# Kernel tuning notes

Hardware: AMD Instinct MI355X
Metric: run time of the kernel (lower is better)

## Reference

```python
import jax, jax.numpy as jnp
import numpy as np

TEMP = 0.5

def setup_inputs() -> dict:
    key = jax.random.key(0)
    k1, k2 = jax.random.split(key)
    B, D = 4096, 256
    x_i = jax.random.normal(k1, (B, D), dtype=jnp.float32)
    x_j = jax.random.normal(k2, (B, D), dtype=jnp.float32)
    return {"x_i": x_i, "x_j": x_j}

def reference(x_i, x_j):
    B = x_i.shape[0]
    z = jnp.concatenate([x_i, x_j], axis=0)  # [2B, D]
    # cosine similarity = normalized dot product (eps matches torch default 1e-8)
    zn = z / jnp.maximum(jnp.linalg.norm(z, axis=-1, keepdims=True), 1e-8)
    sim = zn @ zn.T  # [2B, 2B]
    sim_ij = jnp.diagonal(sim, offset=B)
    sim_ji = jnp.diagonal(sim, offset=-B)
    pos = jnp.concatenate([sim_ij, sim_ji], axis=0)  # [2B]
    # neg_mask = ~eye: zero out self-similarity in the denominator
    exp_sim = jnp.exp(sim / TEMP)
    idx = jnp.arange(2 * B)
    denom = jnp.sum(exp_sim, axis=1) - exp_sim[idx, idx]  # masked row-sum
    loss = jnp.sum(-(pos / TEMP - jnp.log(denom))) / (2 * B)
    return loss
```

## Files before the change

kernel.cpp:

```cpp
#include <hip/hip_runtime.h>
#include <stdint.h>

#define B_ROWS 4096
#define D 256
#define NTOT (2 * B_ROWS)
#define NSPLIT 16
#define BM 256
#define COLS_PER_BLOCK (NTOT / NSPLIT)
#define JT_COUNT (COLS_PER_BLOCK / 64)
#define C_SCALE 2.8853900817779268f

typedef __attribute__((ext_vector_type(8))) short bf16x8;
typedef __attribute__((ext_vector_type(4))) float f32x4;
typedef __attribute__((ext_vector_type(4))) unsigned short us4;

typedef const __attribute__((address_space(1))) char gch;
typedef __attribute__((address_space(3))) char lch;

static __device__ __forceinline__ unsigned short f2bf(float f) {
  union { float f; unsigned u; } v; v.f = f;
  unsigned r = v.u + 0x7FFFu + ((v.u >> 16) & 1u);
  return (unsigned short)(r >> 16);
}

__global__ __launch_bounds__(256) void k_prep(const float* __restrict__ xi,
                                              const float* __restrict__ xj,
                                              unsigned short* __restrict__ zn,
                                              unsigned short* __restrict__ zns,
                                              float* __restrict__ pos,
                                              float* __restrict__ out) {
  if (blockIdx.x == 0 && threadIdx.x == 0) out[0] = 0.0f;
  int p = blockIdx.x * 4 + (threadIdx.x >> 6);
  int lane = threadIdx.x & 63;
  float4 a = ((const float4*)(xi + (size_t)p * D))[lane];
  float4 b = ((const float4*)(xj + (size_t)p * D))[lane];
  float sa = a.x * a.x + a.y * a.y + a.z * a.z + a.w * a.w;
  float sb = b.x * b.x + b.y * b.y + b.z * b.z + b.w * b.w;
  float ab = a.x * b.x + a.y * b.y + a.z * b.z + a.w * b.w;
  #pragma unroll
  for (int m = 1; m < 64; m <<= 1) {
    sa += __shfl_xor(sa, m, 64);
    sb += __shfl_xor(sb, m, 64);
    ab += __shfl_xor(ab, m, 64);
  }
  float ia = 1.0f / fmaxf(sqrtf(sa), 1e-8f);
  float ib = 1.0f / fmaxf(sqrtf(sb), 1e-8f);
  float na[4] = {a.x * ia, a.y * ia, a.z * ia, a.w * ia};
  float nb[4] = {b.x * ib, b.y * ib, b.z * ib, b.w * ib};
  us4 oa, ob, sa4, sb4;
  oa.x = f2bf(na[0]); oa.y = f2bf(na[1]); oa.z = f2bf(na[2]); oa.w = f2bf(na[3]);
  ob.x = f2bf(nb[0]); ob.y = f2bf(nb[1]); ob.z = f2bf(nb[2]); ob.w = f2bf(nb[3]);
  sa4.x = f2bf(na[0] * C_SCALE); sa4.y = f2bf(na[1] * C_SCALE);
  sa4.z = f2bf(na[2] * C_SCALE); sa4.w = f2bf(na[3] * C_SCALE);
  sb4.x = f2bf(nb[0] * C_SCALE); sb4.y = f2bf(nb[1] * C_SCALE);
  sb4.z = f2bf(nb[2] * C_SCALE); sb4.w = f2bf(nb[3] * C_SCALE);
  *(us4*)(zn  + (size_t)p * D + lane * 4) = oa;
  *(us4*)(zn  + (size_t)(p + B_ROWS) * D + lane * 4) = ob;
  *(us4*)(zns + (size_t)p * D + lane * 4) = sa4;
  *(us4*)(zns + (size_t)(p + B_ROWS) * D + lane * 4) = sb4;
  if (lane == 0) {
    float d = ab * ia * ib;
    pos[p] = d;
    pos[p + B_ROWS] = d;
  }
}

__global__ __launch_bounds__(512, 4) void k_gemm(const unsigned short* __restrict__ zn,
                                                 const unsigned short* __restrict__ zns,
                                                 float* __restrict__ part) {
  __shared__ char lds[2 * 32768];
  int rb = (int)(blockIdx.x / NSPLIT) * BM;
  int cs = (int)(blockIdx.x % NSPLIT);
  int cb = cs * COLS_PER_BLOCK;
  int w = threadIdx.x >> 6;
  int lane = threadIdx.x & 63;
  int hi = lane >> 4, lo = lane & 15;

  const char* znb  = (const char*)zn;
  const char* znsb = (const char*)zns;

  bf16x8 a0[8], a1[8];
  int r0 = rb + w * 32 + lo;
  #pragma unroll
  for (int f = 0; f < 8; f++) {
    a0[f] = *(const bf16x8*)(znsb + (size_t)r0 * 512 + f * 64 + hi * 16);
    a1[f] = *(const bf16x8*)(znsb + (size_t)(r0 + 16) * 512 + f * 64 + hi * 16);
  }

  int rdbase[8];
  #pragma unroll
  for (int f = 0; f < 8; f++)
    rdbase[f] = lo * 512 + ((f * 64 + hi * 16) ^ ((lo & 7) << 4));

  float rs[2][4] = {{0.f, 0.f, 0.f, 0.f}, {0.f, 0.f, 0.f, 0.f}};

  auto stage = [&](int bufofs, int colrow) {
    #pragma unroll
    for (int c = 0; c < 4; c++) {
      int local = w * 4096 + c * 1024 + lane * 16;
      int src = local ^ (((local >> 9) & 7) << 4);
      __builtin_amdgcn_global_load_lds(
          (gch*)(znb + (size_t)colrow * 512 + src),
          (lch*)(lds + bufofs + w * 4096 + c * 1024), 16, 0, 0);
    }
  };
  auto compute = [&](int bufofs) {
    #pragma unroll
    for (int nt = 0; nt < 4; nt++) {
      f32x4 acc0 = {0.f, 0.f, 0.f, 0.f}, acc1 = {0.f, 0.f, 0.f, 0.f};
      #pragma unroll
      for (int f = 0; f < 8; f++) {
        bf16x8 b = *(const bf16x8*)(lds + rdbase[f] + bufofs + nt * 8192);
        acc0 = __builtin_amdgcn_mfma_f32_16x16x32_bf16(a0[f], b, acc0, 0, 0, 0);
        acc1 = __builtin_amdgcn_mfma_f32_16x16x32_bf16(a1[f], b, acc1, 0, 0, 0);
      }
      #pragma unroll
      for (int r = 0; r < 4; r++) {
        float e0, e1;
        asm("v_exp_f32 %0, %1" : "=v"(e0) : "v"(acc0[r]));
        asm("v_exp_f32 %0, %1" : "=v"(e1) : "v"(acc1[r]));
        rs[0][r] += e0;
        rs[1][r] += e1;
      }
    }
  };
  auto drain_barrier = []() {
    asm volatile("s_waitcnt vmcnt(0)" ::: "memory");
    __syncthreads();
  };

  stage(0, cb);
  drain_barrier();
  for (int jt = 0; jt < JT_COUNT; jt += 2) {
    if (jt + 1 < JT_COUNT) stage(32768, cb + (jt + 1) * 64);
    compute(0);
    drain_barrier();
    if (jt + 2 < JT_COUNT) stage(0, cb + (jt + 2) * 64);
    compute(32768);
    drain_barrier();
  }

  #pragma unroll
  for (int m = 1; m < 16; m <<= 1) {
    #pragma unroll
    for (int t = 0; t < 2; t++)
      #pragma unroll
      for (int r = 0; r < 4; r++)
        rs[t][r] += __shfl_xor(rs[t][r], m, 64);
  }
  if (lo == 0) {
    #pragma unroll
    for (int t = 0; t < 2; t++)
      #pragma unroll
      for (int r = 0; r < 4; r++)
        part[(size_t)cs * NTOT + rb + w * 32 + t * 16 + hi * 4 + r] = rs[t][r];
  }
}

__global__ __launch_bounds__(256) void k_final(const float* __restrict__ part,
                                               const float* __restrict__ pos,
                                               float* __restrict__ out) {
  int i = blockIdx.x * 256 + threadIdx.x;
  float s = 0.f;
  #pragma unroll
  for (int c = 0; c < NSPLIT; c++) s += part[(size_t)c * NTOT + i];
  float denom = s - 7.3890560989306495f;
  float t = __logf(denom) - 2.0f * pos[i];
  #pragma unroll
  for (int m = 1; m < 64; m <<= 1) t += __shfl_xor(t, m, 64);
  __shared__ float wsum[4];
  int w = threadIdx.x >> 6, lane = threadIdx.x & 63;
  if (lane == 0) wsum[w] = t;
  __syncthreads();
  if (threadIdx.x == 0)
    atomicAdd(out, (wsum[0] + wsum[1] + wsum[2] + wsum[3]) * (1.0f / NTOT));
}

extern "C" void kernel_launch(void* const* d_in, const int* in_sizes, int n_in,
                              void* d_out, int out_size, void* d_ws, size_t ws_size,
                              hipStream_t stream) {
  const float* xi = (const float*)d_in[0];
  const float* xj = (const float*)d_in[1];

  unsigned short* zn  = (unsigned short*)d_ws;
  unsigned short* zns = zn + (size_t)NTOT * D;
  char* base = (char*)(zns + (size_t)NTOT * D);
  float* part = (float*)base;
  float* pos  = (float*)(base + (size_t)NSPLIT * NTOT * 4);

  k_prep<<<B_ROWS / 4, 256, 0, stream>>>(xi, xj, zn, zns, pos, (float*)d_out);
  k_gemm<<<(NTOT / BM) * NSPLIT, 512, 0, stream>>>(zn, zns, part);
  k_final<<<NTOT / 256, 256, 0, stream>>>(part, pos, (float*)d_out);
}
```

Baseline: 100.3 us.

## Fuse final reduction into GEMM via atomics and last-block pattern, drop scaled copy

Removes the separate scaled bf16 copy (zns) and applies the 1/T·log2e scale inside the exp instead, halving the prep kernel's writes. The GEMM now uses 256-thread blocks with 128 rows and 32-column tiles, with a simpler single-tile ping-pong loop. Per-row partial sums are atomically added into a rowsum buffer, and the last block to finish (found through a global counter) computes the log terms and the final loss. This drops the third kernel launch. The cost is float atomics with nondeterministic summation order, an extra multiply per exp, and smaller tiles that reuse each staged B tile across fewer rows.

```diff
diff --git a/kernel.cpp b/kernel.cpp
--- a/kernel.cpp
+++ b/kernel.cpp
@@ -5,9 +5,11 @@
 #define D 256
 #define NTOT (2 * B_ROWS)
 #define NSPLIT 16
-#define BM 256
+#define BM 128
 #define COLS_PER_BLOCK (NTOT / NSPLIT)
-#define JT_COUNT (COLS_PER_BLOCK / 64)
+#define TILE_COLS 32
+#define JT_COUNT (COLS_PER_BLOCK / TILE_COLS)
+#define NBLOCKS ((NTOT / BM) * NSPLIT)
 #define C_SCALE 2.8853900817779268f
 
 typedef __attribute__((ext_vector_type(8))) short bf16x8;
@@ -26,10 +28,10 @@
 __global__ __launch_bounds__(256) void k_prep(const float* __restrict__ xi,
                                               const float* __restrict__ xj,
                                               unsigned short* __restrict__ zn,
-                                              unsigned short* __restrict__ zns,
                                               float* __restrict__ pos,
-                                              float* __restrict__ out) {
-  if (blockIdx.x == 0 && threadIdx.x == 0) out[0] = 0.0f;
+                                              float* __restrict__ rowsum,
+                                              unsigned* __restrict__ counter) {
+  if (blockIdx.x == 0 && threadIdx.x == 0) *counter = 0u;
   int p = blockIdx.x * 4 + (threadIdx.x >> 6);
   int lane = threadIdx.x & 63;
   float4 a = ((const float4*)(xi + (size_t)p * D))[lane];
@@ -45,46 +47,42 @@
   }
   float ia = 1.0f / fmaxf(sqrtf(sa), 1e-8f);
   float ib = 1.0f / fmaxf(sqrtf(sb), 1e-8f);
-  float na[4] = {a.x * ia, a.y * ia, a.z * ia, a.w * ia};
-  float nb[4] = {b.x * ib, b.y * ib, b.z * ib, b.w * ib};
-  us4 oa, ob, sa4, sb4;
-  oa.x = f2bf(na[0]); oa.y = f2bf(na[1]); oa.z = f2bf(na[2]); oa.w = f2bf(na[3]);
-  ob.x = f2bf(nb[0]); ob.y = f2bf(nb[1]); ob.z = f2bf(nb[2]); ob.w = f2bf(nb[3]);
-  sa4.x = f2bf(na[0] * C_SCALE); sa4.y = f2bf(na[1] * C_SCALE);
-  sa4.z = f2bf(na[2] * C_SCALE); sa4.w = f2bf(na[3] * C_SCALE);
-  sb4.x = f2bf(nb[0] * C_SCALE); sb4.y = f2bf(nb[1] * C_SCALE);
-  sb4.z = f2bf(nb[2] * C_SCALE); sb4.w = f2bf(nb[3] * C_SCALE);
-  *(us4*)(zn  + (size_t)p * D + lane * 4) = oa;
-  *(us4*)(zn  + (size_t)(p + B_ROWS) * D + lane * 4) = ob;
-  *(us4*)(zns + (size_t)p * D + lane * 4) = sa4;
-  *(us4*)(zns + (size_t)(p + B_ROWS) * D + lane * 4) = sb4;
+  us4 oa, ob;
+  oa.x = f2bf(a.x * ia); oa.y = f2bf(a.y * ia);
+  oa.z = f2bf(a.z * ia); oa.w = f2bf(a.w * ia);
+  ob.x = f2bf(b.x * ib); ob.y = f2bf(b.y * ib);
+  ob.z = f2bf(b.z * ib); ob.w = f2bf(b.w * ib);
+  *(us4*)(zn + (size_t)p * D + lane * 4) = oa;
+  *(us4*)(zn + (size_t)(p + B_ROWS) * D + lane * 4) = ob;
   if (lane == 0) {
     float d = ab * ia * ib;
     pos[p] = d;
     pos[p + B_ROWS] = d;
+    rowsum[p] = 0.0f;
+    rowsum[p + B_ROWS] = 0.0f;
   }
 }
 
-__global__ __launch_bounds__(512, 4) void k_gemm(const unsigned short* __restrict__ zn,
-                                                 const unsigned short* __restrict__ zns,
-                                                 float* __restrict__ part) {
-  __shared__ char lds[2 * 32768];
+__global__ __launch_bounds__(256) void k_gemm(const unsigned short* __restrict__ zn,
+                                              const float* __restrict__ pos,
+                                              float* __restrict__ rowsum,
+                                              unsigned* __restrict__ counter,
+                                              float* __restrict__ out) {
+  __shared__ char lds[2 * TILE_COLS * 512];
   int rb = (int)(blockIdx.x / NSPLIT) * BM;
-  int cs = (int)(blockIdx.x % NSPLIT);
-  int cb = cs * COLS_PER_BLOCK;
+  int cb = (int)(blockIdx.x % NSPLIT) * COLS_PER_BLOCK;
   int w = threadIdx.x >> 6;
   int lane = threadIdx.x & 63;
   int hi = lane >> 4, lo = lane & 15;
 
-  const char* znb  = (const char*)zn;
-  const char* znsb = (const char*)zns;
+  const char* znb = (const char*)zn;
 
   bf16x8 a0[8], a1[8];
   int r0 = rb + w * 32 + lo;
   #pragma unroll
   for (int f = 0; f < 8; f++) {
-    a0[f] = *(const bf16x8*)(znsb + (size_t)r0 * 512 + f * 64 + hi * 16);
-    a1[f] = *(const bf16x8*)(znsb + (size_t)(r0 + 16) * 512 + f * 64 + hi * 16);
+    a0[f] = *(const bf16x8*)(znb + (size_t)r0 * 512 + f * 64 + hi * 16);
+    a1[f] = *(const bf16x8*)(znb + (size_t)(r0 + 16) * 512 + f * 64 + hi * 16);
   }
 
   int rdbase[8];
@@ -96,29 +94,29 @@
 
   auto stage = [&](int bufofs, int colrow) {
     #pragma unroll
-    for (int c = 0; c < 4; c++) {
-      int local = w * 4096 + c * 1024 + lane * 16;
+    for (int it = 0; it < 4; it++) {
+      int local = it * 4096 + w * 1024 + lane * 16;
       int src = local ^ (((local >> 9) & 7) << 4);
       __builtin_amdgcn_global_load_lds(
           (gch*)(znb + (size_t)colrow * 512 + src),
-          (lch*)(lds + bufofs + w * 4096 + c * 1024), 16, 0, 0);
+          (lch*)(lds + bufofs + it * 4096 + w * 1024), 16, 0, 0);
     }
   };
   auto compute = [&](int bufofs) {
     #pragma unroll
-    for (int nt = 0; nt < 4; nt++) {
+    for (int nt = 0; nt < 2; nt++) {
       f32x4 acc0 = {0.f, 0.f, 0.f, 0.f}, acc1 = {0.f, 0.f, 0.f, 0.f};
       #pragma unroll
       for (int f = 0; f < 8; f++) {
-        bf16x8 b = *(const bf16x8*)(lds + rdbase[f] + bufofs + nt * 8192);
+        bf16x8 b = *(const bf16x8*)(lds + bufofs + nt * 8192 + rdbase[f]);
         acc0 = __builtin_amdgcn_mfma_f32_16x16x32_bf16(a0[f], b, acc0, 0, 0, 0);
         acc1 = __builtin_amdgcn_mfma_f32_16x16x32_bf16(a1[f], b, acc1, 0, 0, 0);
       }
       #pragma unroll
       for (int r = 0; r < 4; r++) {
         float e0, e1;
-        asm("v_exp_f32 %0, %1" : "=v"(e0) : "v"(acc0[r]));
-        asm("v_exp_f32 %0, %1" : "=v"(e1) : "v"(acc1[r]));
+        asm("v_exp_f32 %0, %1" : "=v"(e0) : "v"(C_SCALE * acc0[r]));
+        asm("v_exp_f32 %0, %1" : "=v"(e1) : "v"(C_SCALE * acc1[r]));
         rs[0][r] += e0;
         rs[1][r] += e1;
       }
@@ -131,12 +129,9 @@
 
   stage(0, cb);
   drain_barrier();
-  for (int jt = 0; jt < JT_COUNT; jt += 2) {
-    if (jt + 1 < JT_COUNT) stage(32768, cb + (jt + 1) * 64);
-    compute(0);
-    drain_barrier();
-    if (jt + 2 < JT_COUNT) stage(0, cb + (jt + 2) * 64);
-    compute(32768);
+  for (int jt = 0; jt < JT_COUNT; jt++) {
+    if (jt + 1 < JT_COUNT) stage(((jt + 1) & 1) * 16384, cb + (jt + 1) * TILE_COLS);
+    compute((jt & 1) * 16384);
     drain_barrier();
   }
 
@@ -153,27 +148,28 @@
     for (int t = 0; t < 2; t++)
       #pragma unroll
       for (int r = 0; r < 4; r++)
-        part[(size_t)cs * NTOT + rb + w * 32 + t * 16 + hi * 4 + r] = rs[t][r];
+        atomicAdd(&rowsum[rb + w * 32 + t * 16 + hi * 4 + r], rs[t][r]);
   }
-}
 
-__global__ __launch_bounds__(256) void k_final(const float* __restrict__ part,
-                                               const float* __restrict__ pos,
-                                               float* __restrict__ out) {
-  int i = blockIdx.x * 256 + threadIdx.x;
-  float s = 0.f;
-  #pragma unroll
-  for (int c = 0; c < NSPLIT; c++) s += part[(size_t)c * NTOT + i];
-  float denom = s - 7.3890560989306495f;
-  float t = __logf(denom) - 2.0f * pos[i];
-  #pragma unroll
-  for (int m = 1; m < 64; m <<= 1) t += __shfl_xor(t, m, 64);
-  __shared__ float wsum[4];
-  int w = threadIdx.x >> 6, lane = threadIdx.x & 63;
-  if (lane == 0) wsum[w] = t;
+  __threadfence();
+  __shared__ unsigned s_done;
+  if (threadIdx.x == 0) s_done = atomicAdd(counter, 1u);
   __syncthreads();
-  if (threadIdx.x == 0)
-    atomicAdd(out, (wsum[0] + wsum[1] + wsum[2] + wsum[3]) * (1.0f / NTOT));
+  if (s_done == NBLOCKS - 1) {
+    float acc = 0.f;
+    for (int i = threadIdx.x; i < NTOT; i += 256) {
+      float s = __hip_atomic_load(&rowsum[i], __ATOMIC_RELAXED,
+                                  __HIP_MEMORY_SCOPE_AGENT);
+      acc += __logf(s - 7.3890560989306495f) - 2.0f * pos[i];
+    }
+    #pragma unroll
+    for (int m = 1; m < 64; m <<= 1) acc += __shfl_xor(acc, m, 64);
+    __shared__ float red[4];
+    if (lane == 0) red[w] = acc;
+    __syncthreads();
+    if (threadIdx.x == 0)
+      out[0] = (red[0] + red[1] + red[2] + red[3]) * (1.0f / NTOT);
+  }
 }
 
 extern "C" void kernel_launch(void* const* d_in, const int* in_sizes, int n_in,
@@ -182,13 +178,12 @@
   const float* xi = (const float*)d_in[0];
   const float* xj = (const float*)d_in[1];
 
-  unsigned short* zn  = (unsigned short*)d_ws;
-  unsigned short* zns = zn + (size_t)NTOT * D;
-  char* base = (char*)(zns + (size_t)NTOT * D);
-  float* part = (float*)base;
-  float* pos  = (float*)(base + (size_t)NSPLIT * NTOT * 4);
+  unsigned short* zn = (unsigned short*)d_ws;
+  char* base = (char*)(zn + (size_t)NTOT * D);
+  float* rowsum = (float*)base;
+  float* pos = (float*)(base + (size_t)NTOT * 4);
+  unsigned* counter = (unsigned*)(base + (size_t)2 * NTOT * 4);
 
-  k_prep<<<B_ROWS / 4, 256, 0, stream>>>(xi, xj, zn, zns, pos, (float*)d_out);
-  k_gemm<<<(NTOT / BM) * NSPLIT, 512, 0, stream>>>(zn, zns, part);
-  k_final<<<NTOT / 256, 256, 0, stream>>>(part, pos, (float*)d_out);
+  k_prep<<<B_ROWS / 4, 256, 0, stream>>>(xi, xj, zn, pos, rowsum, counter);
+  k_gemm<<<NBLOCKS, 256, 0, stream>>>(zn, pos, rowsum, counter, (float*)d_out);
 }
```

New measurement: 175.9 us. 75.3% more time.
